# Kernel tuning notes

Measured on AMD Instinct MI355X. Metric: run time of the kernel, lower is better.

Reference implementation:

```python
import jax, jax.numpy as jnp
import numpy as np

B, L, DIN = 16, 4096, 1280
DM, N, R, NL = 128, 16, 8, 2  # d_model=d_inner, d_state, dt_rank, num_layers


def setup_inputs() -> dict:
    key = jax.random.key(0)
    ks = jax.random.split(key, 16)
    f = lambda i, shape, s=0.02: jax.random.normal(ks[i], shape, jnp.float32) * s
    return dict(
        x=jax.random.normal(ks[0], (B, L, DIN), jnp.float32),
        ip_w=f(1, (DM, DIN)), ip_b=f(2, (DM,)),
        in_w=f(3, (NL, 2 * DM, DM)),              # in_proj (no bias), out = [x; z]
        conv_w=f(4, (NL, DM, 2), 0.5), conv_b=f(5, (NL, DM)),  # depthwise causal conv, k=2
        xp_w=f(6, (NL, R + 2 * N, DM)),           # x_proj -> [dt; B; C]
        dt_w=f(7, (NL, DM, R), 0.5), dt_b=f(8, (NL, DM)),
        A_log=jnp.broadcast_to(jnp.log(jnp.arange(1, N + 1, dtype=jnp.float32)), (NL, DM, N)),
        Dp=jnp.ones((NL, DM), jnp.float32),
        out_w=f(9, (NL, DM, DM)),
        ln_g=jnp.ones((DM,), jnp.float32), ln_b=jnp.zeros((DM,), jnp.float32),
        c1_w=f(10, (64, DM)), c1_b=f(11, (64,)),
        c2_w=f(12, (2, 64)), c2_b=f(13, (2,)),
    )


def _mamba(x, in_w, conv_w, conv_b, xp_w, dt_w, dt_b, A_log, Dp, out_w):
    # x: [B,L,DM]
    Bsz, Ls, _ = x.shape
    xz = jnp.einsum('bld,ed->ble', x, in_w)          # [B,L,2*DM]
    u, z = jnp.split(xz, 2, axis=-1)                  # each [B,L,DM]
    # causal depthwise conv, kernel size 2: y_t = w0*u_{t-1} + w1*u_t + b
    u_prev = jnp.pad(u, ((0, 0), (1, 0), (0, 0)))[:, :Ls]
    u = jax.nn.silu(u_prev * conv_w[:, 0] + u * conv_w[:, 1] + conv_b)
    proj = jnp.einsum('bld,ed->ble', u, xp_w)         # [B,L,R+2N]
    dt, Bm, Cm = jnp.split(proj, [R, R + N], axis=-1)
    delta = jax.nn.softplus(jnp.einsum('blr,dr->bld', dt, dt_w) + dt_b)  # [B,L,DM]
    A = -jnp.exp(A_log)                               # [DM,N]

    def step(h, inp):
        d_t, b_t, c_t, u_t = inp                      # [B,DM],[B,N],[B,N],[B,DM]
        dA = jnp.exp(d_t[..., None] * A)              # [B,DM,N]
        h = h * dA + (d_t * u_t)[..., None] * b_t[:, None, :]
        y = jnp.einsum('bdn,bn->bd', h, c_t)
        return h, y

    h0 = jnp.zeros((Bsz, DM, N), x.dtype)
    xs = (delta.transpose(1, 0, 2), Bm.transpose(1, 0, 2),
          Cm.transpose(1, 0, 2), u.transpose(1, 0, 2))
    _, ys = jax.lax.scan(step, h0, xs)                # ys: [L,B,DM]
    y = ys.transpose(1, 0, 2) + u * Dp
    y = y * jax.nn.silu(z)
    return jnp.einsum('bld,ed->ble', y, out_w)


def reference(x, ip_w, ip_b, in_w, conv_w, conv_b, xp_w, dt_w, dt_b, A_log, Dp,
              out_w, ln_g, ln_b, c1_w, c1_b, c2_w, c2_b):
    h = jnp.einsum('bli,di->bld', x, ip_w) + ip_b     # input_proj
    for l in range(NL):                               # residual Mamba blocks
        h = h + _mamba(h, in_w[l], conv_w[l], conv_b[l], xp_w[l], dt_w[l],
                       dt_b[l], A_log[l], Dp[l], out_w[l])
    mu = jnp.mean(h, -1, keepdims=True)
    var = jnp.mean((h - mu) ** 2, -1, keepdims=True)
    h = (h - mu) / jnp.sqrt(var + 1e-5) * ln_g + ln_b # LayerNorm
    p = jnp.mean(h, axis=1)                           # mean pool over seq
    p = jax.nn.relu(p @ c1_w.T + c1_b)                # classifier (dropout=eval/no-op)
    return p @ c2_w.T + c2_b                          # [B,2]
```

## Files before the change

kernel.cpp:

```cpp
#include <hip/hip_runtime.h>
#include <hip/hip_bf16.h>
#include <cstdint>

#define B_   16
#define L_   4096
#define DIN_ 1280
#define DM_  128
#define NS_  16
#define RR_  8
#define NL_  2
#define M_   (B_ * L_)
#define NC_  128
#define CL_  (L_ / NC_)

typedef short short8 __attribute__((ext_vector_type(8)));
typedef float f32x4  __attribute__((ext_vector_type(4)));
typedef unsigned short ushort;
typedef ushort ushort4v __attribute__((ext_vector_type(4)));

__device__ __forceinline__ float silu_f(float x) { return x / (1.f + __expf(-x)); }

__device__ __forceinline__ ushort f2bf(float f) {
  union { float f; uint32_t u; } v; v.f = f;
  uint32_t u = v.u;
  u += 0x7fffu + ((u >> 16) & 1u);
  return (ushort)(u >> 16);
}

#define LDK 40

__global__ __launch_bounds__(256) void gemm_mfma(
    const float* __restrict__ A, const float* __restrict__ W,
    const float* __restrict__ bias,
    float* __restrict__ C0, float* __restrict__ C1,
    int M, int Nc, int K, int split, int residual)
{
  __shared__ ushort As[128 * LDK];
  __shared__ ushort Ws[128 * LDK];
  const int tid = threadIdx.x;
  const int n0 = blockIdx.x * 128;
  const int m0 = blockIdx.y * 128;

  const int srow = tid >> 1;
  const int scol = (tid & 1) << 4;
  const float* gA = A + (size_t)(m0 + srow) * K + scol;
  const float* gW = W + (size_t)(n0 + srow) * K + scol;

  const int lane = tid & 63;
  const int wv = tid >> 6;
  const int wm = (wv & 1) * 64, wn = (wv >> 1) * 64;
  const int ln15 = lane & 15, quad = lane >> 4;

  f32x4 acc[4][4];
#pragma unroll
  for (int i = 0; i < 4; ++i)
#pragma unroll
    for (int j = 0; j < 4; ++j) acc[i][j] = (f32x4){0.f, 0.f, 0.f, 0.f};

  float4 fa[4], fw[4];
#pragma unroll
  for (int j = 0; j < 4; ++j) {
    fa[j] = *(const float4*)(gA + j * 4);
    fw[j] = *(const float4*)(gW + j * 4);
  }

  for (int k0 = 0; k0 < K; k0 += 32) {
    __syncthreads();
#pragma unroll
    for (int j = 0; j < 4; ++j) {
      ushort4v a4 = { f2bf(fa[j].x), f2bf(fa[j].y), f2bf(fa[j].z), f2bf(fa[j].w) };
      ushort4v w4 = { f2bf(fw[j].x), f2bf(fw[j].y), f2bf(fw[j].z), f2bf(fw[j].w) };
      *(ushort4v*)&As[srow * LDK + scol + j * 4] = a4;
      *(ushort4v*)&Ws[srow * LDK + scol + j * 4] = w4;
    }
    if (k0 + 32 < K) {
#pragma unroll
      for (int j = 0; j < 4; ++j) {
        fa[j] = *(const float4*)(gA + k0 + 32 + j * 4);
        fw[j] = *(const float4*)(gW + k0 + 32 + j * 4);
      }
    }
    __syncthreads();
    short8 aF[4], bF[4];
#pragma unroll
    for (int mt = 0; mt < 4; ++mt)
      aF[mt] = *(const short8*)&As[(wm + mt * 16 + ln15) * LDK + quad * 8];
#pragma unroll
    for (int nt = 0; nt < 4; ++nt)
      bF[nt] = *(const short8*)&Ws[(wn + nt * 16 + ln15) * LDK + quad * 8];
#pragma unroll
    for (int mt = 0; mt < 4; ++mt)
#pragma unroll
      for (int nt = 0; nt < 4; ++nt)
        acc[mt][nt] = __builtin_amdgcn_mfma_f32_16x16x32_bf16(
            aF[mt], bF[nt], acc[mt][nt], 0, 0, 0);
  }

  const bool left = n0 < split;
#pragma unroll
  for (int mt = 0; mt < 4; ++mt) {
    const int row = m0 + wm + mt * 16 + quad * 4;
#pragma unroll
    for (int nt = 0; nt < 4; ++nt) {
      const int col = n0 + wn + nt * 16 + ln15;
      const float bv = bias ? bias[col] : 0.f;
#pragma unroll
      for (int r = 0; r < 4; ++r) {
        float v = acc[mt][nt][r] + bv;
        if (left) {
          float* p = C0 + (size_t)(row + r) * split + col;
          if (residual) v += *p;
          *p = v;
        } else {
          C1[(size_t)(row + r) * (Nc - split) + (col - split)] = silu_f(v);
        }
      }
    }
  }
}

__global__ __launch_bounds__(256) void xpc(
    const float* __restrict__ uraw,
    const float* __restrict__ cw, const float* __restrict__ cb,
    const float* __restrict__ xpw,
    const float* __restrict__ dtw,
    const float* __restrict__ dtb,
    float* __restrict__ uout,
    float* __restrict__ delta,
    float* __restrict__ BCout)
{
  __shared__ float u_s[32][132];
  __shared__ float xp_s[40 * 128];
  __shared__ float dtw_s[128 * 8];
  __shared__ float dtb_s[128];
  __shared__ float proj_s[32][41];
  const int tid = threadIdx.x;
  const size_t m0 = (size_t)blockIdx.x * 32;
  const int t0 = (int)(m0 & (L_ - 1));

#pragma unroll
  for (int i = 0; i < 16; ++i) {
    int f = tid + i * 256;
    int tok = f >> 7, dd = f & 127;
    float cur = uraw[(m0 + tok) * DM_ + dd];
    float prev = (t0 + tok > 0) ? uraw[(m0 + tok - 1) * DM_ + dd] : 0.f;
    float v = silu_f(cw[dd * 2] * prev + cw[dd * 2 + 1] * cur + cb[dd]);
    u_s[tok][dd] = v;
    uout[(m0 + tok) * DM_ + dd] = v;
  }
  for (int f = tid; f < 40 * 128; f += 256) xp_s[f] = xpw[f];
  for (int f = tid; f < 128 * 8; f += 256) dtw_s[f] = dtw[f];
  if (tid < 128) dtb_s[tid] = dtb[tid];
  __syncthreads();

  {
    const int tok = tid & 31, eg = tid >> 5;
    float pa[5] = {0.f, 0.f, 0.f, 0.f, 0.f};
    for (int dd = 0; dd < 128; dd += 4) {
      float4 uu = *(const float4*)&u_s[tok][dd];
#pragma unroll
      for (int i = 0; i < 5; ++i) {
        float4 xv = *(const float4*)&xp_s[(eg * 5 + i) * 128 + dd];
        pa[i] += uu.x * xv.x + uu.y * xv.y + uu.z * xv.z + uu.w * xv.w;
      }
    }
#pragma unroll
    for (int i = 0; i < 5; ++i) proj_s[tok][eg * 5 + i] = pa[i];
  }
  __syncthreads();

#pragma unroll
  for (int i = 0; i < 4; ++i) {
    int f = tid + i * 256;
    BCout[m0 * 32 + f] = proj_s[f >> 5][8 + (f & 31)];
  }

  {
    const int tok = tid & 31, dg = tid >> 5;
    float pr[8];
#pragma unroll
    for (int r = 0; r < 8; ++r) pr[r] = proj_s[tok][r];
#pragma unroll
    for (int jj = 0; jj < 16; ++jj) {
      int dd = dg * 16 + jj;
      float acc = dtb_s[dd];
#pragma unroll
      for (int r = 0; r < 8; ++r) acc += pr[r] * dtw_s[dd * 8 + r];
      float sp = (acc > 20.f) ? acc : log1pf(__expf(acc));
      u_s[tok][dd] = sp;
    }
  }
  __syncthreads();
#pragma unroll
  for (int i = 0; i < 16; ++i) {
    int f = tid + i * 256;
    delta[(m0 + (f >> 7)) * DM_ + (f & 127)] = u_s[f >> 7][f & 127];
  }
}

__global__ __launch_bounds__(128) void scan_h(
    const float* __restrict__ delta, const float* __restrict__ u,
    const float* __restrict__ BC, const float* __restrict__ alog,
    float* __restrict__ hend, float* __restrict__ Ssum)
{
  const int d = threadIdx.x;
  const int chunk = blockIdx.x, b = blockIdx.y;
  float a[NS_], h[NS_];
#pragma unroll
  for (int n = 0; n < NS_; ++n) {
    a[n] = -__expf(alog[d * NS_ + n]);
    h[n] = 0.f;
  }
  float S = 0.f;
  const size_t rowbase = (size_t)b * L_ + (size_t)chunk * CL_;
  float dlt = delta[rowbase * DM_ + d];
  float uu  = u[rowbase * DM_ + d];
  for (int s = 0; s < CL_; ++s) {
    const float* Brow = BC + (rowbase + s) * 32;
    float Bv[NS_];
#pragma unroll
    for (int n = 0; n < NS_; ++n) Bv[n] = Brow[n];
    float dn = 0.f, un = 0.f;
    if (s + 1 < CL_) {
      dn = delta[(rowbase + s + 1) * DM_ + d];
      un = u[(rowbase + s + 1) * DM_ + d];
    }
    const float du = dlt * uu;
    S += dlt;
#pragma unroll
    for (int n = 0; n < NS_; ++n) {
      float dA = __expf(dlt * a[n]);
      h[n] = fmaf(h[n], dA, du * Bv[n]);
    }
    dlt = dn; uu = un;
  }
  const size_t o = ((size_t)b * NC_ + chunk) * DM_ + d;
  float4* hp = (float4*)(hend + o * NS_);
#pragma unroll
  for (int q = 0; q < 4; ++q)
    hp[q] = make_float4(h[q * 4], h[q * 4 + 1], h[q * 4 + 2], h[q * 4 + 3]);
  Ssum[o] = S;
}

__global__ __launch_bounds__(256) void scan_comb(
    const float* __restrict__ hend, const float* __restrict__ Ssum,
    const float* __restrict__ alog, float* __restrict__ hstart)
{
  const int idx = blockIdx.x * 256 + threadIdx.x;
  const int n = idx & 15;
  const int d = (idx >> 4) & 127;
  const int b = idx >> 11;
  const float a = -__expf(alog[d * NS_ + n]);
  float hs = 0.f;
  for (int c = 0; c < NC_; ++c) {
    const size_t o = ((size_t)b * NC_ + c) * DM_ + d;
    hstart[o * NS_ + n] = hs;
    hs = hend[o * NS_ + n] + __expf(a * Ssum[o]) * hs;
  }
}

__global__ __launch_bounds__(128) void scan_y(
    const float* __restrict__ delta, const float* __restrict__ u,
    const float* __restrict__ zbuf, const float* __restrict__ BC,
    const float* __restrict__ alog, const float* __restrict__ Dpv,
    const float* __restrict__ hstart, float* __restrict__ y)
{
  const int d = threadIdx.x;
  const int chunk = blockIdx.x, b = blockIdx.y;
  float a[NS_], h[NS_];
  const size_t o = ((size_t)b * NC_ + chunk) * DM_ + d;
  const float4* hp = (const float4*)(hstart + o * NS_);
#pragma unroll
  for (int q = 0; q < 4; ++q) {
    float4 v = hp[q];
    h[q * 4] = v.x; h[q * 4 + 1] = v.y; h[q * 4 + 2] = v.z; h[q * 4 + 3] = v.w;
  }
#pragma unroll
  for (int n = 0; n < NS_; ++n) a[n] = -__expf(alog[d * NS_ + n]);
  const float Dd = Dpv[d];
  const size_t rowbase = (size_t)b * L_ + (size_t)chunk * CL_;
  float dlt = delta[rowbase * DM_ + d];
  float uu  = u[rowbase * DM_ + d];
  float zz  = zbuf[rowbase * DM_ + d];
  for (int s = 0; s < CL_; ++s) {
    const float* Brow = BC + (rowbase + s) * 32;
    float Bv[NS_], Cv[NS_];
#pragma unroll
    for (int n = 0; n < NS_; ++n) { Bv[n] = Brow[n]; Cv[n] = Brow[16 + n]; }
    float dn = 0.f, un = 0.f, zn = 0.f;
    if (s + 1 < CL_) {
      dn = delta[(rowbase + s + 1) * DM_ + d];
      un = u[(rowbase + s + 1) * DM_ + d];
      zn = zbuf[(rowbase + s + 1) * DM_ + d];
    }
    const float du = dlt * uu;
    float yv = uu * Dd;
#pragma unroll
    for (int n = 0; n < NS_; ++n) {
      float dA = __expf(dlt * a[n]);
      h[n] = fmaf(h[n], dA, du * Bv[n]);
      yv = fmaf(h[n], Cv[n], yv);
    }
    y[(rowbase + s) * DM_ + d] = yv * zz;
    dlt = dn; uu = un; zz = zn;
  }
}

__global__ __launch_bounds__(256) void lnpool1(
    const float* __restrict__ h, float* __restrict__ partial)
{
  const int b = blockIdx.y, ch = blockIdx.x;
  const int tid = threadIdx.x, wave = tid >> 6, lane = tid & 63;
  float a0 = 0.f, a1 = 0.f;
  const int tbase = ch * 256 + wave * 64;
  for (int i = 0; i < 64; ++i) {
    const float* row = h + ((size_t)b * L_ + tbase + i) * DM_;
    float x0 = row[lane], x1 = row[lane + 64];
    float s = x0 + x1, sq = x0 * x0 + x1 * x1;
    for (int off = 32; off; off >>= 1) { s += __shfl_xor(s, off); sq += __shfl_xor(sq, off); }
    float mu = s * (1.f / 128.f);
    float var = sq * (1.f / 128.f) - mu * mu;
    float rstd = rsqrtf(var + 1e-5f);
    a0 += (x0 - mu) * rstd;
    a1 += (x1 - mu) * rstd;
  }
  __shared__ float ps[4][128];
  ps[wave][lane] = a0;
  ps[wave][lane + 64] = a1;
  __syncthreads();
  if (tid < 128)
    partial[((size_t)b * 16 + ch) * DM_ + tid] = ps[0][tid] + ps[1][tid] + ps[2][tid] + ps[3][tid];
}

__global__ __launch_bounds__(256) void headk(
    const float* __restrict__ partial,
    const float* __restrict__ lng, const float* __restrict__ lnb,
    const float* __restrict__ c1w, const float* __restrict__ c1b,
    const float* __restrict__ c2w, const float* __restrict__ c2b,
    float* __restrict__ out)
{
  __shared__ float pool[16][128];
  __shared__ float p1[16][64];
  const int tid = threadIdx.x;
  for (int i = tid; i < 16 * 128; i += 256) {
    int b = i >> 7, dd = i & 127;
    float s = 0.f;
    for (int c = 0; c < 16; ++c) s += partial[((size_t)b * 16 + c) * DM_ + dd];
    pool[b][dd] = s * (1.f / (float)L_) * lng[dd] + lnb[dd];
  }
  __syncthreads();
  for (int i = tid; i < 16 * 64; i += 256) {
    int b = i >> 6, j = i & 63;
    float acc = c1b[j];
    for (int dd = 0; dd < 128; ++dd) acc += pool[b][dd] * c1w[j * 128 + dd];
    p1[b][j] = fmaxf(acc, 0.f);
  }
  __syncthreads();
  if (tid < 32) {
    int b = tid >> 1, k = tid & 1;
    float acc = c2b[k];
    for (int j = 0; j < 64; ++j) acc += p1[b][j] * c2w[k * 64 + j];
    out[b * 2 + k] = acc;
  }
}

extern "C" void kernel_launch(void* const* d_in, const int* in_sizes, int n_in,
                              void* d_out, int out_size, void* d_ws, size_t ws_size,
                              hipStream_t stream)
{
  (void)in_sizes; (void)n_in; (void)out_size; (void)ws_size;
  const float* x    = (const float*)d_in[0];
  const float* ipw  = (const float*)d_in[1];
  const float* ipb  = (const float*)d_in[2];
  const float* inw  = (const float*)d_in[3];
  const float* cw   = (const float*)d_in[4];
  const float* cb   = (const float*)d_in[5];
  const float* xpw  = (const float*)d_in[6];
  const float* dtw  = (const float*)d_in[7];
  const float* dtb  = (const float*)d_in[8];
  const float* alog = (const float*)d_in[9];
  const float* Dpv  = (const float*)d_in[10];
  const float* outw = (const float*)d_in[11];
  const float* lng  = (const float*)d_in[12];
  const float* lnb  = (const float*)d_in[13];
  const float* c1w  = (const float*)d_in[14];
  const float* c1b  = (const float*)d_in[15];
  const float* c2w  = (const float*)d_in[16];
  const float* c2b  = (const float*)d_in[17];

  float* ws = (float*)d_ws;
  const size_t SZ = (size_t)M_ * DM_;
  float* h      = ws;
  float* yraw   = h + SZ;
  float* zbuf   = yraw + SZ;
  float* ubuf   = zbuf + SZ;
  float* dbuf   = ubuf + SZ;
  float* bc     = dbuf + SZ;
  float* hend   = bc + (size_t)M_ * 32;
  float* hstart = hend + (size_t)B_ * NC_ * DM_ * NS_;
  float* Ssum   = hstart + (size_t)B_ * NC_ * DM_ * NS_;
  float* part   = Ssum + (size_t)B_ * NC_ * DM_;

  gemm_mfma<<<dim3(1, M_ / 128), 256, 0, stream>>>(
      x, ipw, ipb, h, nullptr, M_, DM_, DIN_, DM_, 0);

  for (int l = 0; l < NL_; ++l) {
    gemm_mfma<<<dim3(2, M_ / 128), 256, 0, stream>>>(
        h, inw + (size_t)l * 256 * DM_, nullptr, yraw, zbuf, M_, 256, DM_, DM_, 0);
    xpc<<<M_ / 32, 256, 0, stream>>>(
        yraw, cw + l * DM_ * 2, cb + l * DM_,
        xpw + l * 40 * DM_, dtw + l * DM_ * RR_, dtb + l * DM_,
        ubuf, dbuf, bc);
    scan_h<<<dim3(NC_, B_), 128, 0, stream>>>(
        dbuf, ubuf, bc, alog + l * DM_ * NS_, hend, Ssum);
    scan_comb<<<(B_ * DM_ * NS_) / 256, 256, 0, stream>>>(
        hend, Ssum, alog + l * DM_ * NS_, hstart);
    scan_y<<<dim3(NC_, B_), 128, 0, stream>>>(
        dbuf, ubuf, zbuf, bc, alog + l * DM_ * NS_, Dpv + l * DM_, hstart, yraw);
    gemm_mfma<<<dim3(1, M_ / 128), 256, 0, stream>>>(
        yraw, outw + (size_t)l * DM_ * DM_, nullptr, h, nullptr, M_, DM_, DM_, DM_, 1);
  }

  lnpool1<<<dim3(16, B_), 256, 0, stream>>>(h, part);
  headk<<<1, 256, 0, stream>>>(part, lng, lnb, c1w, c1b, c2w, c2b, (float*)d_out);
}
```

Measured before the change: 915.7 us.

## Store intermediate activations and weights in bf16 to halve memory traffic

Every intermediate activation buffer (hidden state, u, z, delta, B/C, y) is now stored as bf16 instead of fp32. Weights are converted to bf16 once by a new kernel, so the GEMMs load bf16 tiles directly and skip per-tile conversion. This cuts the bandwidth of the memory-bound scan, conv and GEMM stages. In exchange, the residual stream is also accumulated in bf16, which adds rounding error across layers.

```diff
diff --git a/kernel.cpp b/kernel.cpp
--- a/kernel.cpp
+++ b/kernel.cpp
@@ -27,12 +27,32 @@
   return (ushort)(u >> 16);
 }
 
+__device__ __forceinline__ float bf2f(ushort u) {
+  union { uint32_t u; float f; } v; v.u = ((uint32_t)u) << 16; return v.f;
+}
+
+__global__ __launch_bounds__(256) void wcvt_k(
+    const float* __restrict__ a, int na,
+    const float* __restrict__ b, int nb,
+    const float* __restrict__ c, int nc,
+    ushort* __restrict__ dst)
+{
+  int i = blockIdx.x * 256 + threadIdx.x;
+  float v;
+  if (i < na) v = a[i];
+  else if (i < na + nb) v = b[i - na];
+  else if (i < na + nb + nc) v = c[i - na - nb];
+  else return;
+  dst[i] = f2bf(v);
+}
+
 #define LDK 40
 
-__global__ __launch_bounds__(256) void gemm_mfma(
-    const float* __restrict__ A, const float* __restrict__ W,
+template<int AF32>
+__global__ __launch_bounds__(256) void gemm_bf(
+    const void* __restrict__ Av, const ushort* __restrict__ W,
     const float* __restrict__ bias,
-    float* __restrict__ C0, float* __restrict__ C1,
+    ushort* __restrict__ C0, ushort* __restrict__ C1,
     int M, int Nc, int K, int split, int residual)
 {
   __shared__ ushort As[128 * LDK];
@@ -43,8 +63,9 @@
 
   const int srow = tid >> 1;
   const int scol = (tid & 1) << 4;
-  const float* gA = A + (size_t)(m0 + srow) * K + scol;
-  const float* gW = W + (size_t)(n0 + srow) * K + scol;
+  const ushort* gW  = W + (size_t)(n0 + srow) * K + scol;
+  const float*  gAf = (const float*)Av + (size_t)(m0 + srow) * K + scol;
+  const ushort* gAb = (const ushort*)Av + (size_t)(m0 + srow) * K + scol;
 
   const int lane = tid & 63;
   const int wv = tid >> 6;
@@ -57,28 +78,42 @@
 #pragma unroll
     for (int j = 0; j < 4; ++j) acc[i][j] = (f32x4){0.f, 0.f, 0.f, 0.f};
 
-  float4 fa[4], fw[4];
-#pragma unroll
-  for (int j = 0; j < 4; ++j) {
-    fa[j] = *(const float4*)(gA + j * 4);
-    fw[j] = *(const float4*)(gW + j * 4);
-  }
+  float4 fa[4];
+  short8 a2[2], w2[2];
+  if constexpr (AF32) {
+#pragma unroll
+    for (int j = 0; j < 4; ++j) fa[j] = *(const float4*)(gAf + j * 4);
+  } else {
+    a2[0] = *(const short8*)gAb;
+    a2[1] = *(const short8*)(gAb + 8);
+  }
+  w2[0] = *(const short8*)gW;
+  w2[1] = *(const short8*)(gW + 8);
 
   for (int k0 = 0; k0 < K; k0 += 32) {
     __syncthreads();
-#pragma unroll
-    for (int j = 0; j < 4; ++j) {
-      ushort4v a4 = { f2bf(fa[j].x), f2bf(fa[j].y), f2bf(fa[j].z), f2bf(fa[j].w) };
-      ushort4v w4 = { f2bf(fw[j].x), f2bf(fw[j].y), f2bf(fw[j].z), f2bf(fw[j].w) };
-      *(ushort4v*)&As[srow * LDK + scol + j * 4] = a4;
-      *(ushort4v*)&Ws[srow * LDK + scol + j * 4] = w4;
-    }
+    if constexpr (AF32) {
+#pragma unroll
+      for (int j = 0; j < 4; ++j) {
+        ushort4v a4 = { f2bf(fa[j].x), f2bf(fa[j].y), f2bf(fa[j].z), f2bf(fa[j].w) };
+        *(ushort4v*)&As[srow * LDK + scol + j * 4] = a4;
+      }
+    } else {
+      *(short8*)&As[srow * LDK + scol]     = a2[0];
+      *(short8*)&As[srow * LDK + scol + 8] = a2[1];
+    }
+    *(short8*)&Ws[srow * LDK + scol]     = w2[0];
+    *(short8*)&Ws[srow * LDK + scol + 8] = w2[1];
     if (k0 + 32 < K) {
-#pragma unroll
-      for (int j = 0; j < 4; ++j) {
-        fa[j] = *(const float4*)(gA + k0 + 32 + j * 4);
-        fw[j] = *(const float4*)(gW + k0 + 32 + j * 4);
+      if constexpr (AF32) {
+#pragma unroll
+        for (int j = 0; j < 4; ++j) fa[j] = *(const float4*)(gAf + k0 + 32 + j * 4);
+      } else {
+        a2[0] = *(const short8*)(gAb + k0 + 32);
+        a2[1] = *(const short8*)(gAb + k0 + 40);
       }
+      w2[0] = *(const short8*)(gW + k0 + 32);
+      w2[1] = *(const short8*)(gW + k0 + 40);
     }
     __syncthreads();
     short8 aF[4], bF[4];
@@ -108,11 +143,11 @@
       for (int r = 0; r < 4; ++r) {
         float v = acc[mt][nt][r] + bv;
         if (left) {
-          float* p = C0 + (size_t)(row + r) * split + col;
-          if (residual) v += *p;
-          *p = v;
+          ushort* p = C0 + (size_t)(row + r) * split + col;
+          if (residual) v += bf2f(*p);
+          *p = f2bf(v);
         } else {
-          C1[(size_t)(row + r) * (Nc - split) + (col - split)] = silu_f(v);
+          C1[(size_t)(row + r) * (Nc - split) + (col - split)] = f2bf(silu_f(v));
         }
       }
     }
@@ -120,14 +155,14 @@
 }
 
 __global__ __launch_bounds__(256) void xpc(
-    const float* __restrict__ uraw,
+    const ushort* __restrict__ uraw,
     const float* __restrict__ cw, const float* __restrict__ cb,
     const float* __restrict__ xpw,
     const float* __restrict__ dtw,
     const float* __restrict__ dtb,
-    float* __restrict__ uout,
-    float* __restrict__ delta,
-    float* __restrict__ BCout)
+    ushort* __restrict__ uout,
+    ushort* __restrict__ delta,
+    ushort* __restrict__ BCout)
 {
   __shared__ float u_s[32][132];
   __shared__ float xp_s[40 * 128];
@@ -142,11 +177,11 @@
   for (int i = 0; i < 16; ++i) {
     int f = tid + i * 256;
     int tok = f >> 7, dd = f & 127;
-    float cur = uraw[(m0 + tok) * DM_ + dd];
-    float prev = (t0 + tok > 0) ? uraw[(m0 + tok - 1) * DM_ + dd] : 0.f;
+    float cur = bf2f(uraw[(m0 + tok) * DM_ + dd]);
+    float prev = (t0 + tok > 0) ? bf2f(uraw[(m0 + tok - 1) * DM_ + dd]) : 0.f;
     float v = silu_f(cw[dd * 2] * prev + cw[dd * 2 + 1] * cur + cb[dd]);
     u_s[tok][dd] = v;
-    uout[(m0 + tok) * DM_ + dd] = v;
+    uout[(m0 + tok) * DM_ + dd] = f2bf(v);
   }
   for (int f = tid; f < 40 * 128; f += 256) xp_s[f] = xpw[f];
   for (int f = tid; f < 128 * 8; f += 256) dtw_s[f] = dtw[f];
@@ -172,7 +207,7 @@
 #pragma unroll
   for (int i = 0; i < 4; ++i) {
     int f = tid + i * 256;
-    BCout[m0 * 32 + f] = proj_s[f >> 5][8 + (f & 31)];
+    BCout[m0 * 32 + f] = f2bf(proj_s[f >> 5][8 + (f & 31)]);
   }
 
   {
@@ -194,13 +229,13 @@
 #pragma unroll
   for (int i = 0; i < 16; ++i) {
     int f = tid + i * 256;
-    delta[(m0 + (f >> 7)) * DM_ + (f & 127)] = u_s[f >> 7][f & 127];
+    delta[(m0 + (f >> 7)) * DM_ + (f & 127)] = f2bf(u_s[f >> 7][f & 127]);
   }
 }
 
 __global__ __launch_bounds__(128) void scan_h(
-    const float* __restrict__ delta, const float* __restrict__ u,
-    const float* __restrict__ BC, const float* __restrict__ alog,
+    const ushort* __restrict__ delta, const ushort* __restrict__ u,
+    const ushort* __restrict__ BC, const float* __restrict__ alog,
     float* __restrict__ hend, float* __restrict__ Ssum)
 {
   const int d = threadIdx.x;
@@ -213,17 +248,21 @@
   }
   float S = 0.f;
   const size_t rowbase = (size_t)b * L_ + (size_t)chunk * CL_;
-  float dlt = delta[rowbase * DM_ + d];
-  float uu  = u[rowbase * DM_ + d];
+  float dlt = bf2f(delta[rowbase * DM_ + d]);
+  float uu  = bf2f(u[rowbase * DM_ + d]);
   for (int s = 0; s < CL_; ++s) {
-    const float* Brow = BC + (rowbase + s) * 32;
+    const uint32_t* Br = (const uint32_t*)(BC + (rowbase + s) * 32);
     float Bv[NS_];
 #pragma unroll
-    for (int n = 0; n < NS_; ++n) Bv[n] = Brow[n];
+    for (int q = 0; q < 8; ++q) {
+      uint32_t w = Br[q];
+      Bv[2 * q]     = __uint_as_float(w << 16);
+      Bv[2 * q + 1] = __uint_as_float(w & 0xffff0000u);
+    }
     float dn = 0.f, un = 0.f;
     if (s + 1 < CL_) {
-      dn = delta[(rowbase + s + 1) * DM_ + d];
-      un = u[(rowbase + s + 1) * DM_ + d];
+      dn = bf2f(delta[(rowbase + s + 1) * DM_ + d]);
+      un = bf2f(u[(rowbase + s + 1) * DM_ + d]);
     }
     const float du = dlt * uu;
     S += dlt;
@@ -260,10 +299,10 @@
 }
 
 __global__ __launch_bounds__(128) void scan_y(
-    const float* __restrict__ delta, const float* __restrict__ u,
-    const float* __restrict__ zbuf, const float* __restrict__ BC,
+    const ushort* __restrict__ delta, const ushort* __restrict__ u,
+    const ushort* __restrict__ zbuf, const ushort* __restrict__ BC,
     const float* __restrict__ alog, const float* __restrict__ Dpv,
-    const float* __restrict__ hstart, float* __restrict__ y)
+    const float* __restrict__ hstart, ushort* __restrict__ y)
 {
   const int d = threadIdx.x;
   const int chunk = blockIdx.x, b = blockIdx.y;
@@ -279,19 +318,25 @@
   for (int n = 0; n < NS_; ++n) a[n] = -__expf(alog[d * NS_ + n]);
   const float Dd = Dpv[d];
   const size_t rowbase = (size_t)b * L_ + (size_t)chunk * CL_;
-  float dlt = delta[rowbase * DM_ + d];
-  float uu  = u[rowbase * DM_ + d];
-  float zz  = zbuf[rowbase * DM_ + d];
+  float dlt = bf2f(delta[rowbase * DM_ + d]);
+  float uu  = bf2f(u[rowbase * DM_ + d]);
+  float zz  = bf2f(zbuf[rowbase * DM_ + d]);
   for (int s = 0; s < CL_; ++s) {
-    const float* Brow = BC + (rowbase + s) * 32;
+    const uint32_t* Br = (const uint32_t*)(BC + (rowbase + s) * 32);
     float Bv[NS_], Cv[NS_];
 #pragma unroll
-    for (int n = 0; n < NS_; ++n) { Bv[n] = Brow[n]; Cv[n] = Brow[16 + n]; }
+    for (int q = 0; q < 8; ++q) {
+      uint32_t wB = Br[q], wC = Br[8 + q];
+      Bv[2 * q]     = __uint_as_float(wB << 16);
+      Bv[2 * q + 1] = __uint_as_float(wB & 0xffff0000u);
+      Cv[2 * q]     = __uint_as_float(wC << 16);
+      Cv[2 * q + 1] = __uint_as_float(wC & 0xffff0000u);
+    }
     float dn = 0.f, un = 0.f, zn = 0.f;
     if (s + 1 < CL_) {
-      dn = delta[(rowbase + s + 1) * DM_ + d];
-      un = u[(rowbase + s + 1) * DM_ + d];
-      zn = zbuf[(rowbase + s + 1) * DM_ + d];
+      dn = bf2f(delta[(rowbase + s + 1) * DM_ + d]);
+      un = bf2f(u[(rowbase + s + 1) * DM_ + d]);
+      zn = bf2f(zbuf[(rowbase + s + 1) * DM_ + d]);
     }
     const float du = dlt * uu;
     float yv = uu * Dd;
@@ -301,21 +346,21 @@
       h[n] = fmaf(h[n], dA, du * Bv[n]);
       yv = fmaf(h[n], Cv[n], yv);
     }
-    y[(rowbase + s) * DM_ + d] = yv * zz;
+    y[(rowbase + s) * DM_ + d] = f2bf(yv * zz);
     dlt = dn; uu = un; zz = zn;
   }
 }
 
 __global__ __launch_bounds__(256) void lnpool1(
-    const float* __restrict__ h, float* __restrict__ partial)
+    const ushort* __restrict__ h, float* __restrict__ partial)
 {
   const int b = blockIdx.y, ch = blockIdx.x;
   const int tid = threadIdx.x, wave = tid >> 6, lane = tid & 63;
   float a0 = 0.f, a1 = 0.f;
   const int tbase = ch * 256 + wave * 64;
   for (int i = 0; i < 64; ++i) {
-    const float* row = h + ((size_t)b * L_ + tbase + i) * DM_;
-    float x0 = row[lane], x1 = row[lane + 64];
+    const ushort* row = h + ((size_t)b * L_ + tbase + i) * DM_;
+    float x0 = bf2f(row[lane]), x1 = bf2f(row[lane + 64]);
     float s = x0 + x1, sq = x0 * x0 + x1 * x1;
     for (int off = 32; off; off >>= 1) { s += __shfl_xor(s, off); sq += __shfl_xor(sq, off); }
     float mu = s * (1.f / 128.f);
@@ -388,39 +433,53 @@
   const float* c2w  = (const float*)d_in[16];
   const float* c2b  = (const float*)d_in[17];
 
-  float* ws = (float*)d_ws;
-  const size_t SZ = (size_t)M_ * DM_;
-  float* h      = ws;
-  float* yraw   = h + SZ;
-  float* zbuf   = yraw + SZ;
-  float* ubuf   = zbuf + SZ;
-  float* dbuf   = ubuf + SZ;
-  float* bc     = dbuf + SZ;
-  float* hend   = bc + (size_t)M_ * 32;
-  float* hstart = hend + (size_t)B_ * NC_ * DM_ * NS_;
-  float* Ssum   = hstart + (size_t)B_ * NC_ * DM_ * NS_;
+  const size_t SZ  = (size_t)M_ * DM_;
+  const size_t HSZ = (size_t)B_ * NC_ * DM_ * NS_;
+
+  ushort* us   = (ushort*)d_ws;
+  ushort* hb   = us;
+  ushort* uraw = hb + SZ;
+  ushort* zb   = uraw + SZ;
+  ushort* ub   = zb + SZ;
+  ushort* db   = ub + SZ;
+  ushort* bcb  = db + SZ;
+  ushort* wb   = bcb + (size_t)M_ * 32;
+  const int NIP = DM_ * DIN_;
+  const int NIN = NL_ * 2 * DM_ * DM_;
+  const int NOW = NL_ * DM_ * DM_;
+  ushort* wip  = wb;
+  ushort* win  = wb + NIP;
+  ushort* wout = win + NIN;
+
+  float* fs     = (float*)(wb + (NIP + NIN + NOW));
+  float* hend   = fs;
+  float* hstart = hend + HSZ;
+  float* Ssum   = hstart + HSZ;
   float* part   = Ssum + (size_t)B_ * NC_ * DM_;
 
-  gemm_mfma<<<dim3(1, M_ / 128), 256, 0, stream>>>(
-      x, ipw, ipb, h, nullptr, M_, DM_, DIN_, DM_, 0);
+  wcvt_k<<<(NIP + NIN + NOW + 255) / 256, 256, 0, stream>>>(
+      ipw, NIP, inw, NIN, outw, NOW, wb);
+
+  gemm_bf<1><<<dim3(1, M_ / 128), 256, 0, stream>>>(
+      x, wip, ipb, hb, nullptr, M_, DM_, DIN_, DM_, 0);
 
   for (int l = 0; l < NL_; ++l) {
-    gemm_mfma<<<dim3(2, M_ / 128), 256, 0, stream>>>(
-        h, inw + (size_t)l * 256 * DM_, nullptr, yraw, zbuf, M_, 256, DM_, DM_, 0);
+    gemm_bf<0><<<dim3(2, M_ / 128), 256, 0, stream>>>(
+        hb, win + (size_t)l * 2 * DM_ * DM_, nullptr, uraw, zb, M_, 256, DM_, DM_, 0);
     xpc<<<M_ / 32, 256, 0, stream>>>(
-        yraw, cw + l * DM_ * 2, cb + l * DM_,
+        uraw, cw + l * DM_ * 2, cb + l * DM_,
         xpw + l * 40 * DM_, dtw + l * DM_ * RR_, dtb + l * DM_,
-        ubuf, dbuf, bc);
+        ub, db, bcb);
     scan_h<<<dim3(NC_, B_), 128, 0, stream>>>(
-        dbuf, ubuf, bc, alog + l * DM_ * NS_, hend, Ssum);
+        db, ub, bcb, alog + l * DM_ * NS_, hend, Ssum);
     scan_comb<<<(B_ * DM_ * NS_) / 256, 256, 0, stream>>>(
         hend, Ssum, alog + l * DM_ * NS_, hstart);
     scan_y<<<dim3(NC_, B_), 128, 0, stream>>>(
-        dbuf, ubuf, zbuf, bc, alog + l * DM_ * NS_, Dpv + l * DM_, hstart, yraw);
-    gemm_mfma<<<dim3(1, M_ / 128), 256, 0, stream>>>(
-        yraw, outw + (size_t)l * DM_ * DM_, nullptr, h, nullptr, M_, DM_, DM_, DM_, 1);
-  }
-
-  lnpool1<<<dim3(16, B_), 256, 0, stream>>>(h, part);
+        db, ub, zb, bcb, alog + l * DM_ * NS_, Dpv + l * DM_, hstart, uraw);
+    gemm_bf<0><<<dim3(1, M_ / 128), 256, 0, stream>>>(
+        uraw, wout + (size_t)l * DM_ * DM_, nullptr, hb, nullptr, M_, DM_, DM_, DM_, 1);
+  }
+
+  lnpool1<<<dim3(16, B_), 256, 0, stream>>>(hb, part);
   headk<<<1, 256, 0, stream>>>(part, lng, lnb, c1w, c1b, c2w, c2b, (float*)d_out);
 }
```

Result: faster. 886.3 us (-3.2%).
